# Kernel tuning notes

Hardware: AMD Instinct MI355X
Metric: run time of the kernel (lower is better)

## Reference

```python
import jax, jax.numpy as jnp
import numpy as np
import math

C = 256
GROUPS = 8
EPS = 1e-5

def setup_inputs() -> dict:
    key = jax.random.key(0)
    ks = jax.random.split(key, 10)
    b, c, h, w = 4, C, 64, 64
    x = jax.random.normal(ks[0], (b, c, h, w), dtype=jnp.float32)
    scale = 1.0 / math.sqrt(c)
    wq = jax.random.normal(ks[1], (c, c), dtype=jnp.float32) * scale
    wk = jax.random.normal(ks[2], (c, c), dtype=jnp.float32) * scale
    wv = jax.random.normal(ks[3], (c, c), dtype=jnp.float32) * scale
    wp = jax.random.normal(ks[4], (c, c), dtype=jnp.float32) * scale
    bq = jnp.zeros((c,), jnp.float32)
    bk = jnp.zeros((c,), jnp.float32)
    bv = jnp.zeros((c,), jnp.float32)
    bp = jnp.zeros((c,), jnp.float32)
    gamma = jnp.ones((c,), jnp.float32)
    beta = jnp.zeros((c,), jnp.float32)
    return {"x": x, "gamma": gamma, "beta": beta, "wq": wq, "bq": bq,
            "wk": wk, "bk": bk, "wv": wv, "bv": bv, "wp": wp, "bp": bp}

def _group_norm(x, gamma, beta):
    b, c, h, w = x.shape
    xr = x.reshape(b, GROUPS, c // GROUPS, h, w)
    mean = xr.mean(axis=(2, 3, 4), keepdims=True)
    var = xr.var(axis=(2, 3, 4), keepdims=True)
    xn = ((xr - mean) * jax.lax.rsqrt(var + EPS)).reshape(b, c, h, w)
    return xn * gamma[None, :, None, None] + beta[None, :, None, None]

def _conv1x1(x, w, bias):
    # 1x1 conv == channel matmul: [b,c,h,w] x [out,in] -> [b,out,h,w]
    return jnp.einsum('bchw,dc->bdhw', x, w) + bias[None, :, None, None]

def reference(x, gamma, beta, wq, bq, wk, bk, wv, bv, wp, bp):
    b, c, h, w = x.shape
    residual = x
    xn = _group_norm(x, gamma, beta)
    q = _conv1x1(xn, wq, bq).reshape(b, c, h * w).transpose(0, 2, 1)  # [b, hw, c]
    k = _conv1x1(xn, wk, bk).reshape(b, c, h * w)                    # [b, c, hw]
    v = _conv1x1(xn, wv, bv).reshape(b, c, h * w).transpose(0, 2, 1)  # [b, hw, c]
    attn = jnp.einsum('bqc,bck->bqk', q, k) / jnp.sqrt(jnp.float32(c))
    attn = jax.nn.softmax(attn, axis=-1)
    out = jnp.einsum('bqk,bkc->bqc', attn, v)                         # [b, hw, c]
    out = out.transpose(0, 2, 1).reshape(b, c, h, w)
    out = _conv1x1(out, wp, bp)
    return out + residual
```

## Files before the change

### kernel.cpp

```cpp
#include <hip/hip_runtime.h>

#define HW 4096
#define CD 256
#define KB 32
#define NKB 32
#define NSP 4
#define C1 0.09016844f

typedef __bf16 bf16x8v __attribute__((ext_vector_type(8)));
typedef float f32x4 __attribute__((ext_vector_type(4)));
typedef unsigned short u16;
typedef unsigned int u32;
typedef u16 u16x4 __attribute__((ext_vector_type(4)));
typedef u16 u16x8 __attribute__((ext_vector_type(8)));

static __device__ __forceinline__ u16 f2bf(float f){
  __bf16 h = (__bf16)f;
  return __builtin_bit_cast(u16, h);
}
static __device__ __forceinline__ float bf2f(u16 v){
  u32 u = ((u32)v) << 16;
  return __builtin_bit_cast(float, u);
}

static __device__ __forceinline__ f32x4 MFMA(u16x8 a, u16x8 b, f32x4 c){
  return __builtin_amdgcn_mfma_f32_16x16x32_bf16(
      __builtin_bit_cast(bf16x8v, a), __builtin_bit_cast(bf16x8v, b), c, 0, 0, 0);
}

#define GLL16(gsrc, ldst) __builtin_amdgcn_global_load_lds( \
    (const __attribute__((address_space(1))) void*)(gsrc),  \
    (__attribute__((address_space(3))) void*)(ldst), 16, 0, 0)

__global__ void k_prep(const float* __restrict__ wq, const float* __restrict__ wk,
                       const float* __restrict__ wv, const float* __restrict__ wp,
                       u16* __restrict__ Wbf){
  int z = blockIdx.y;
  const float* src = (z==0)?wq:(z==1)?wk:(z==2)?wv:wp;
  int i = (blockIdx.x*256 + threadIdx.x)*4;
  float4 v = *(const float4*)(src + i);
  u16x4 o = { f2bf(v.x), f2bf(v.y), f2bf(v.z), f2bf(v.w) };
  *(u16x4*)(Wbf + z*65536 + i) = o;
}

__global__ void k_gn1(const float* __restrict__ x, float* __restrict__ gpart){
  int g = blockIdx.x, b = blockIdx.y, ck = blockIdx.z;
  int tid = threadIdx.x;
  const float* xp = x + ((size_t)(b*CD) + g*32)*HW + ck*512;
  float s0 = 0.f, s1 = 0.f;
  #pragma unroll
  for (int j = 0; j < 16; ++j){
    int idx = j*1024 + tid*4;
    float4 v = *(const float4*)(xp + (size_t)(idx >> 9)*HW + (idx & 511));
    s0 += v.x + v.y + v.z + v.w;
    s1 += v.x*v.x + v.y*v.y + v.z*v.z + v.w*v.w;
  }
  #pragma unroll
  for (int m = 1; m < 64; m <<= 1){ s0 += __shfl_xor(s0, m); s1 += __shfl_xor(s1, m); }
  __shared__ float red[8];
  int lane = tid & 63, wave = tid >> 6;
  if (lane == 0){ red[wave] = s0; red[4+wave] = s1; }
  __syncthreads();
  if (tid == 0){
    float* dst = gpart + ((b*8 + g)*8 + ck)*2;
    dst[0] = red[0]+red[1]+red[2]+red[3];
    dst[1] = red[4]+red[5]+red[6]+red[7];
  }
}

__global__ void k_gn2(const float* __restrict__ x, const float* __restrict__ gamma,
                      const float* __restrict__ beta, const float* __restrict__ gpart,
                      u16* __restrict__ xnT){
  int g = blockIdx.x, b = blockIdx.y, ck = blockIdx.z;
  int tid = threadIdx.x;
  float s0 = 0.f, s1 = 0.f;
  #pragma unroll
  for (int s = 0; s < 8; ++s){
    const float* p = gpart + ((b*8 + g)*8 + s)*2;
    s0 += p[0]; s1 += p[1];
  }
  float inv_n = 1.0f/(32.0f*HW);
  float mean = s0*inv_n;
  float var = s1*inv_n - mean*mean;
  float rstd = rsqrtf(var + 1e-5f);
  int pl = tid >> 2, c8 = (tid & 3)*8;
  float av[8], bv_[8];
  #pragma unroll
  for (int e = 0; e < 8; ++e){
    int c = g*32 + c8 + e;
    float a = rstd * gamma[c];
    av[e] = a;
    bv_[e] = beta[c] - mean*a;
  }
  const float* xb = x + (size_t)(b*CD + g*32 + c8)*HW;
  #pragma unroll
  for (int it = 0; it < 8; ++it){
    int p = ck*512 + it*64 + pl;
    u16x8 o;
    #pragma unroll
    for (int e = 0; e < 8; ++e){
      float v = xb[(size_t)e*HW + p];
      o[e] = f2bf(v*av[e] + bv_[e]);
    }
    *(u16x8*)(xnT + ((size_t)(b*HW) + p)*CD + g*32 + c8) = o;
  }
}

__global__ __launch_bounds__(256,2) void k_qkv(const u16* __restrict__ xnT, const u16* __restrict__ Wbf,
    const float* __restrict__ bq, const float* __restrict__ bk, const float* __restrict__ bv,
    u16* __restrict__ Q, u16* __restrict__ K, u16* __restrict__ V){
  __shared__ u16 tile[4][4096];
  int z = blockIdx.z, b = blockIdx.y, pbase = blockIdx.x*64;
  int tid = threadIdx.x, lane = tid & 63, wave = tid >> 6;
  int lq = lane & 15, lg = lane >> 4;
  const u16* W = Wbf + z*65536;
  const float* bias = (z==0)?bq:(z==1)?bk:bv;
  int nbase = wave*64;
  f32x4 acc[4][4] = {};
  #pragma unroll
  for (int kk = 0; kk < 8; ++kk){
    u16x8 af[4], bf[4];
    #pragma unroll
    for (int m = 0; m < 4; ++m)
      af[m] = *(const u16x8*)(xnT + ((size_t)(b*HW + pbase + m*16 + lq))*CD + kk*32 + lg*8);
    #pragma unroll
    for (int n = 0; n < 4; ++n)
      bf[n] = *(const u16x8*)(W + (size_t)(nbase + n*16 + lq)*CD + kk*32 + lg*8);
    #pragma unroll
    for (int m = 0; m < 4; ++m)
      #pragma unroll
      for (int n = 0; n < 4; ++n)
        acc[m][n] = MFMA(af[m], bf[n], acc[m][n]);
  }
  #pragma unroll
  for (int n = 0; n < 4; ++n){
    float bb = bias[nbase + n*16 + lq];
    #pragma unroll
    for (int m = 0; m < 4; ++m){
      acc[m][n][0] += bb; acc[m][n][1] += bb; acc[m][n][2] += bb; acc[m][n][3] += bb;
    }
  }
  if (z == 2){
    #pragma unroll
    for (int m = 0; m < 4; ++m)
      #pragma unroll
      for (int n = 0; n < 4; ++n){
        int d = nbase + n*16 + lq;
        int p0 = pbase + m*16 + lg*4;
        u16x4 o = { f2bf(acc[m][n][0]), f2bf(acc[m][n][1]), f2bf(acc[m][n][2]), f2bf(acc[m][n][3]) };
        *(u16x4*)(V + (size_t)(b*CD + d)*HW + p0) = o;
      }
  } else {
    u16* dst = (z==0)?Q:K;
    u16* tl = tile[wave];
    #pragma unroll
    for (int m = 0; m < 4; ++m)
      #pragma unroll
      for (int n = 0; n < 4; ++n)
        #pragma unroll
        for (int r = 0; r < 4; ++r){
          int row = m*16 + lg*4 + r;
          int col = n*16 + lq;
          tl[row*64 + ((((col>>3) + row) & 7)<<3) + (col & 7)] = f2bf(acc[m][n][r]);
        }
    #pragma unroll
    for (int j = 0; j < 8; ++j){
      int idx = j*64 + lane;
      int row = idx >> 3, ch = idx & 7;
      u16x8 v = *(const u16x8*)(tl + row*64 + (((ch + row)&7)<<3));
      *(u16x8*)(dst + ((size_t)(b*HW + pbase + row))*CD + nbase + ch*8) = v;
    }
  }
}

__global__ __launch_bounds__(256,3) void k_attn(const u16* __restrict__ Q, const u16* __restrict__ K,
    const u16* __restrict__ V, u16* __restrict__ Opart, float2* __restrict__ ml){
  extern __shared__ char smem[];
  int tid = threadIdx.x, lane = tid & 63, wave = tid >> 6;
  int lq = lane & 15, lg = lane >> 4;
  int qt = blockIdx.x, sp = blockIdx.y, b = blockIdx.z;
  int qbase = qt*64 + wave*16;
  int key0 = sp*(NKB*KB);

  int ke[4], ve[4];
  #pragma unroll
  for (int i = 0; i < 4; ++i){
    int G = i*256 + tid;
    int kr = G >> 5;
    ke[i] = kr*CD + (((G & 31) ^ kr) & 31)*8;
    int vrow = G >> 3;
    int p = (G >> 2) & 1;
    int j = ((G & 3) - vrow) & 3;
    ve[i] = (vrow*2 + p)*HW + j*8;
  }
  int bvo = (lq>>1)*128 + (((lq&1)*4 + ((lg + (lq>>1)) & 3)))*16;

  u16x8 qa[8];
  #pragma unroll
  for (int cc = 0; cc < 8; ++cc)
    qa[cc] = *(const u16x8*)(Q + ((size_t)(b*HW + qbase + lq))*CD + cc*32 + lg*8);

  f32x4 o[16] = {};
  float m_ = -3.0e38f, l_ = 0.f;

  const u16* Kb = K + (size_t)(b*HW + key0)*CD;
  const u16* Vb = V + (size_t)(b*CD)*HW + key0;
  char* vd = smem + 32768;
  char* Pw = smem + 49152 + wave*1024;

  {
    char* kd = smem;
    #pragma unroll
    for (int i = 0; i < 4; ++i){
      GLL16(Kb + ke[i], kd + i*4096 + wave*1024);
      GLL16(Vb + ve[i], vd + i*4096 + wave*1024);
    }
  }
  __syncthreads();
  int cur = 0;
  for (int kb = 0; kb < NKB; ++kb){
    if (kb + 1 < NKB){
      char* kd = smem + (cur^1)*16384;
      const u16* kg = Kb + (size_t)(kb+1)*KB*CD;
      #pragma unroll
      for (int i = 0; i < 4; ++i)
        GLL16(kg + ke[i], kd + i*4096 + wave*1024);
    }
    const char* kt = smem + cur*16384;

    f32x4 sa[2];
    sa[0] = (f32x4){0.f,0.f,0.f,0.f};
    sa[1] = (f32x4){0.f,0.f,0.f,0.f};
    #pragma unroll
    for (int nt = 0; nt < 2; ++nt){
      int row = nt*16 + lq;
      #pragma unroll
      for (int cc = 0; cc < 8; ++cc){
        int ch = cc*4 + lg;
        u16x8 kf = *(const u16x8*)(kt + row*512 + (((ch ^ row) & 31) << 4));
        sa[nt] = MFMA(kf, qa[cc], sa[nt]);
      }
    }
    float v = fmaxf(fmaxf(fmaxf(sa[0][0], sa[0][1]), fmaxf(sa[0][2], sa[0][3])),
                    fmaxf(fmaxf(sa[1][0], sa[1][1]), fmaxf(sa[1][2], sa[1][3]))) * C1;
    v = fmaxf(v, __shfl_xor(v, 16));
    v = fmaxf(v, __shfl_xor(v, 32));
    if (!__all(v <= m_ + 8.0f)){
      float nm = fmaxf(m_, v);
      float corr = exp2f(m_ - nm);
      m_ = nm;
      l_ *= corr;
      float cr[4];
      #pragma unroll
      for (int r = 0; r < 4; ++r)
        cr[r] = __shfl(corr, lg*4 + r);
      #pragma unroll
      for (int nf = 0; nf < 16; ++nf)
        #pragma unroll
        for (int r = 0; r < 4; ++r)
          o[nf][r] *= cr[r];
    }
    float rs = 0.f;
    u32 pw[4];
    #pragma unroll
    for (int w = 0; w < 4; ++w){
      int nt = w >> 1, rr = w & 1;
      float p0 = exp2f(sa[nt][2*rr]  *C1 - m_);
      float p1 = exp2f(sa[nt][2*rr+1]*C1 - m_);
      rs += p0 + p1;
      pw[w] = (u32)f2bf(p0) | ((u32)f2bf(p1) << 16);
    }
    rs += __shfl_xor(rs, 16);
    rs += __shfl_xor(rs, 32);
    l_ += rs;
    #pragma unroll
    for (int w = 0; w < 4; ++w){
      int chunk = 2*(w>>1) + (lg>>1);
      int slot  = (chunk + (lq>>1)) & 3;
      int addr  = (lq>>1)*128 + ((lq&1)*4 + slot)*16 + ((2*lg + (w&1))&3)*4;
      *(u32*)(Pw + addr) = pw[w];
    }
    __syncthreads();
    u16x8 pa = *(const u16x8*)(Pw + bvo);
    #pragma unroll
    for (int nf = 0; nf < 16; ++nf){
      u16x8 vf = *(const u16x8*)(vd + nf*1024 + bvo);
      o[nf] = MFMA(pa, vf, o[nf]);
    }
    __syncthreads();
    if (kb + 1 < NKB){
      const u16* vg = Vb + (kb+1)*KB;
      #pragma unroll
      for (int i = 0; i < 4; ++i)
        GLL16(vg + ve[i], vd + i*4096 + wave*1024);
    }
    cur ^= 1;
  }
  size_t ob = ((size_t)((sp*4 + b)*HW + qbase))*CD;
  #pragma unroll
  for (int nf = 0; nf < 16; ++nf){
    int c = nf*16 + lq;
    #pragma unroll
    for (int r = 0; r < 4; ++r){
      int qq = lg*4 + r;
      Opart[ob + (size_t)qq*CD + c] = f2bf(o[nf][r]);
    }
  }
  if (lg == 0){
    ml[(size_t)(sp*4 + b)*HW + qbase + lq] = make_float2(m_, l_);
  }
}

__global__ void k_comb(const u16* __restrict__ Opart, const float2* __restrict__ ml,
                       u16* __restrict__ Opm){
  int b = blockIdx.y;
  int q = blockIdx.x*8 + (threadIdx.x >> 5);
  int c0 = (threadIdx.x & 31)*8;
  float2 e[NSP];
  float m = -3.0e38f;
  #pragma unroll
  for (int s = 0; s < NSP; ++s){
    e[s] = ml[(size_t)(s*4 + b)*HW + q];
    m = fmaxf(m, e[s].x);
  }
  float w[NSP], den = 0.f;
  #pragma unroll
  for (int s = 0; s < NSP; ++s){
    w[s] = exp2f(e[s].x - m);
    den += e[s].y * w[s];
  }
  float inv = 1.0f / den;
  float sum[8] = {};
  #pragma unroll
  for (int s = 0; s < NSP; ++s){
    u16x8 v = *(const u16x8*)(Opart + ((size_t)((s*4 + b)*HW) + q)*CD + c0);
    float ws = w[s];
    #pragma unroll
    for (int t = 0; t < 8; ++t)
      sum[t] += bf2f(v[t]) * ws;
  }
  u16x8 o;
  #pragma unroll
  for (int t = 0; t < 8; ++t)
    o[t] = f2bf(sum[t]*inv);
  *(u16x8*)(Opm + ((size_t)(b*HW) + q)*CD + c0) = o;
}

__global__ __launch_bounds__(256,2) void k_proj(const u16* __restrict__ Opm, const u16* __restrict__ Wp,
    const float* __restrict__ bp, const float* __restrict__ x, float* __restrict__ out){
  int b = blockIdx.y, pbase = blockIdx.x*64;
  int tid = threadIdx.x, lane = tid & 63, wave = tid >> 6;
  int lq = lane & 15, lg = lane >> 4;
  int nbase = wave*64;
  f32x4 acc[4][4] = {};
  #pragma unroll
  for (int kk = 0; kk < 8; ++kk){
    u16x8 af[4], bf[4];
    #pragma unroll
    for (int m = 0; m < 4; ++m)
      af[m] = *(const u16x8*)(Opm + ((size_t)(b*HW + pbase + m*16 + lq))*CD + kk*32 + lg*8);
    #pragma unroll
    for (int n = 0; n < 4; ++n)
      bf[n] = *(const u16x8*)(Wp + (size_t)(nbase + n*16 + lq)*CD + kk*32 + lg*8);
    #pragma unroll
    for (int m = 0; m < 4; ++m)
      #pragma unroll
      for (int n = 0; n < 4; ++n)
        acc[m][n] = MFMA(af[m], bf[n], acc[m][n]);
  }
  #pragma unroll
  for (int m = 0; m < 4; ++m)
    #pragma unroll
    for (int n = 0; n < 4; ++n){
      int d = nbase + n*16 + lq;
      int p0 = pbase + m*16 + lg*4;
      size_t base = (size_t)(b*CD + d)*HW + p0;
      float bb = bp[d];
      float4 res = *(const float4*)(x + base);
      float4 ov;
      ov.x = acc[m][n][0] + bb + res.x;
      ov.y = acc[m][n][1] + bb + res.y;
      ov.z = acc[m][n][2] + bb + res.z;
      ov.w = acc[m][n][3] + bb + res.w;
      *(float4*)(out + base) = ov;
    }
}

extern "C" void kernel_launch(void* const* d_in, const int* in_sizes, int n_in,
                              void* d_out, int out_size, void* d_ws, size_t ws_size,
                              hipStream_t stream){
  const float* x     = (const float*)d_in[0];
  const float* gamma = (const float*)d_in[1];
  const float* beta  = (const float*)d_in[2];
  const float* wq    = (const float*)d_in[3];
  const float* bq    = (const float*)d_in[4];
  const float* wk    = (const float*)d_in[5];
  const float* bk    = (const float*)d_in[6];
  const float* wv    = (const float*)d_in[7];
  const float* bv    = (const float*)d_in[8];
  const float* wp    = (const float*)d_in[9];
  const float* bp    = (const float*)d_in[10];
  float* out = (float*)d_out;

  char* ws = (char*)d_ws;
  u16*   xnT   = (u16*)(ws);
  u16*   Qb    = (u16*)(ws + (8ull<<20));
  u16*   Kb    = (u16*)(ws + (16ull<<20));
  u16*   Vb    = (u16*)(ws + (24ull<<20));
  u16*   Opm   = (u16*)(ws + (32ull<<20));
  u16*   Wbf   = (u16*)(ws + (40ull<<20));
  float2* mlb  = (float2*)(ws + (40ull<<20) + (512ull<<10));
  u16*   Opart = (u16*)(ws + (41ull<<20));
  float* gpart = (float*)Qb;

  hipFuncSetAttribute((const void*)k_attn, hipFuncAttributeMaxDynamicSharedMemorySize, 53248);

  k_prep<<<dim3(64,4), 256, 0, stream>>>(wq, wk, wv, wp, Wbf);
  k_gn1 <<<dim3(8,4,8), 256, 0, stream>>>(x, gpart);
  k_gn2 <<<dim3(8,4,8), 256, 0, stream>>>(x, gamma, beta, gpart, xnT);
  k_qkv <<<dim3(64,4,3), 256, 0, stream>>>(xnT, Wbf, bq, bk, bv, Qb, Kb, Vb);
  k_attn<<<dim3(64,NSP,4), 256, 53248, stream>>>(Qb, Kb, Vb, Opart, mlb);
  k_comb<<<dim3(512,4), 256, 0, stream>>>(Opart, mlb, Opm);
  k_proj<<<dim3(64,4), 256, 0, stream>>>(Opm, Wbf + 3*65536, bp, x, out);
}
```

Before: 187.9 us.

## Split attention work across wave pairs with double-buffered V and deferred rescale

The attention kernel moves from 256 to 512 threads. Each pair of waves shares 16 queries, with one wave handling half of every 32-key block for QK^T and half of the 256 output channels for PV. V is now double-buffered alongside K, so each iteration needs one barrier instead of two. The running-max rescale is deferred until after the PV MFMAs, using a row max shared through LDS and a lazy threshold starting from m=0. This halves per-wave accumulator registers and raises waves per CU, at the cost of more LDS per block, cross-wave max/sum exchange, and some overflow risk if early scores are far above zero.

```diff
diff --git a/kernel.cpp b/kernel.cpp
--- a/kernel.cpp
+++ b/kernel.cpp
@@ -173,19 +173,20 @@
   }
 }
 
-__global__ __launch_bounds__(256,3) void k_attn(const u16* __restrict__ Q, const u16* __restrict__ K,
+__global__ __launch_bounds__(512,4) void k_attn(const u16* __restrict__ Q, const u16* __restrict__ K,
     const u16* __restrict__ V, u16* __restrict__ Opart, float2* __restrict__ ml){
   extern __shared__ char smem[];
   int tid = threadIdx.x, lane = tid & 63, wave = tid >> 6;
   int lq = lane & 15, lg = lane >> 4;
+  int pair = wave >> 1, half = wave & 1;
   int qt = blockIdx.x, sp = blockIdx.y, b = blockIdx.z;
-  int qbase = qt*64 + wave*16;
+  int qbase = qt*64 + pair*16;
   int key0 = sp*(NKB*KB);
 
-  int ke[4], ve[4];
-  #pragma unroll
-  for (int i = 0; i < 4; ++i){
-    int G = i*256 + tid;
+  int ke[2], ve[2];
+  #pragma unroll
+  for (int i = 0; i < 2; ++i){
+    int G = i*512 + tid;
     int kr = G >> 5;
     ke[i] = kr*CD + (((G & 31) ^ kr) & 31)*8;
     int vrow = G >> 3;
@@ -200,20 +201,20 @@
   for (int cc = 0; cc < 8; ++cc)
     qa[cc] = *(const u16x8*)(Q + ((size_t)(b*HW + qbase + lq))*CD + cc*32 + lg*8);
 
-  f32x4 o[16] = {};
-  float m_ = -3.0e38f, l_ = 0.f;
+  f32x4 o[8] = {};
+  float m_ = 0.f, l_ = 0.f;
 
   const u16* Kb = K + (size_t)(b*HW + key0)*CD;
   const u16* Vb = V + (size_t)(b*CD)*HW + key0;
-  char* vd = smem + 32768;
-  char* Pw = smem + 49152 + wave*1024;
+  char* Pw = smem + 65536 + pair*1024;
+  float* mb = (float*)(smem + 69632);
 
   {
-    char* kd = smem;
-    #pragma unroll
-    for (int i = 0; i < 4; ++i){
-      GLL16(Kb + ke[i], kd + i*4096 + wave*1024);
-      GLL16(Vb + ve[i], vd + i*4096 + wave*1024);
+    char* kd = smem; char* vd = smem + 32768;
+    #pragma unroll
+    for (int i = 0; i < 2; ++i){
+      GLL16(Kb + ke[i], kd + i*8192 + wave*1024);
+      GLL16(Vb + ve[i], vd + i*8192 + wave*1024);
     }
   }
   __syncthreads();
@@ -223,30 +224,58 @@
       char* kd = smem + (cur^1)*16384;
       const u16* kg = Kb + (size_t)(kb+1)*KB*CD;
       #pragma unroll
-      for (int i = 0; i < 4; ++i)
-        GLL16(kg + ke[i], kd + i*4096 + wave*1024);
+      for (int i = 0; i < 2; ++i)
+        GLL16(kg + ke[i], kd + i*8192 + wave*1024);
     }
     const char* kt = smem + cur*16384;
 
-    f32x4 sa[2];
-    sa[0] = (f32x4){0.f,0.f,0.f,0.f};
-    sa[1] = (f32x4){0.f,0.f,0.f,0.f};
-    #pragma unroll
-    for (int nt = 0; nt < 2; ++nt){
-      int row = nt*16 + lq;
-      #pragma unroll
-      for (int cc = 0; cc < 8; ++cc){
-        int ch = cc*4 + lg;
-        u16x8 kf = *(const u16x8*)(kt + row*512 + (((ch ^ row) & 31) << 4));
-        sa[nt] = MFMA(kf, qa[cc], sa[nt]);
-      }
-    }
-    float v = fmaxf(fmaxf(fmaxf(sa[0][0], sa[0][1]), fmaxf(sa[0][2], sa[0][3])),
-                    fmaxf(fmaxf(sa[1][0], sa[1][1]), fmaxf(sa[1][2], sa[1][3]))) * C1;
+    f32x4 sa = (f32x4){0.f,0.f,0.f,0.f};
+    int row = half*16 + lq;
+    #pragma unroll
+    for (int cc = 0; cc < 8; ++cc){
+      int ch = cc*4 + lg;
+      u16x8 kf = *(const u16x8*)(kt + row*512 + (((ch ^ row) & 31) << 4));
+      sa = MFMA(kf, qa[cc], sa);
+    }
+    float t0 = sa[0]*C1, t1 = sa[1]*C1, t2 = sa[2]*C1, t3 = sa[3]*C1;
+    float v = fmaxf(fmaxf(t0, t1), fmaxf(t2, t3));
     v = fmaxf(v, __shfl_xor(v, 16));
     v = fmaxf(v, __shfl_xor(v, 32));
-    if (!__all(v <= m_ + 8.0f)){
-      float nm = fmaxf(m_, v);
+    if (lg == 0) mb[pair*32 + half*16 + lq] = v;
+    float rs;
+    {
+      float p0 = exp2f(t0 - m_), p1 = exp2f(t1 - m_);
+      float p2 = exp2f(t2 - m_), p3 = exp2f(t3 - m_);
+      rs = (p0 + p1) + (p2 + p3);
+      u32 w0 = (u32)f2bf(p0) | ((u32)f2bf(p1) << 16);
+      u32 w1 = (u32)f2bf(p2) | ((u32)f2bf(p3) << 16);
+      int chunk = 2*half + (lg>>1);
+      int slot  = (chunk + (lq>>1)) & 3;
+      int base  = (lq>>1)*128 + ((lq&1)*4 + slot)*16;
+      *(u32*)(Pw + base + ((2*lg + 0)&3)*4) = w0;
+      *(u32*)(Pw + base + ((2*lg + 1)&3)*4) = w1;
+    }
+    rs += __shfl_xor(rs, 16);
+    rs += __shfl_xor(rs, 32);
+    l_ += rs;
+    __syncthreads();
+    if (kb + 1 < NKB){
+      char* vd = smem + 32768 + (cur^1)*16384;
+      const u16* vg = Vb + (kb+1)*KB;
+      #pragma unroll
+      for (int i = 0; i < 2; ++i)
+        GLL16(vg + ve[i], vd + i*8192 + wave*1024);
+    }
+    float mx = fmaxf(mb[pair*32 + lq], mb[pair*32 + 16 + lq]);
+    u16x8 pa = *(const u16x8*)(Pw + bvo);
+    const char* vt = smem + 32768 + cur*16384;
+    #pragma unroll
+    for (int f = 0; f < 8; ++f){
+      u16x8 vf = *(const u16x8*)(vt + (half*8 + f)*1024 + bvo);
+      o[f] = MFMA(pa, vf, o[f]);
+    }
+    if (!__all(mx <= m_ + 8.0f)){
+      float nm = fmaxf(m_, mx);
       float corr = exp2f(m_ - nm);
       m_ = nm;
       l_ *= corr;
@@ -255,60 +284,27 @@
       for (int r = 0; r < 4; ++r)
         cr[r] = __shfl(corr, lg*4 + r);
       #pragma unroll
-      for (int nf = 0; nf < 16; ++nf)
+      for (int f = 0; f < 8; ++f)
         #pragma unroll
         for (int r = 0; r < 4; ++r)
-          o[nf][r] *= cr[r];
-    }
-    float rs = 0.f;
-    u32 pw[4];
-    #pragma unroll
-    for (int w = 0; w < 4; ++w){
-      int nt = w >> 1, rr = w & 1;
-      float p0 = exp2f(sa[nt][2*rr]  *C1 - m_);
-      float p1 = exp2f(sa[nt][2*rr+1]*C1 - m_);
-      rs += p0 + p1;
-      pw[w] = (u32)f2bf(p0) | ((u32)f2bf(p1) << 16);
-    }
-    rs += __shfl_xor(rs, 16);
-    rs += __shfl_xor(rs, 32);
-    l_ += rs;
-    #pragma unroll
-    for (int w = 0; w < 4; ++w){
-      int chunk = 2*(w>>1) + (lg>>1);
-      int slot  = (chunk + (lq>>1)) & 3;
-      int addr  = (lq>>1)*128 + ((lq&1)*4 + slot)*16 + ((2*lg + (w&1))&3)*4;
-      *(u32*)(Pw + addr) = pw[w];
-    }
-    __syncthreads();
-    u16x8 pa = *(const u16x8*)(Pw + bvo);
-    #pragma unroll
-    for (int nf = 0; nf < 16; ++nf){
-      u16x8 vf = *(const u16x8*)(vd + nf*1024 + bvo);
-      o[nf] = MFMA(pa, vf, o[nf]);
-    }
-    __syncthreads();
-    if (kb + 1 < NKB){
-      const u16* vg = Vb + (kb+1)*KB;
-      #pragma unroll
-      for (int i = 0; i < 4; ++i)
-        GLL16(vg + ve[i], vd + i*4096 + wave*1024);
+          o[f][r] *= cr[r];
     }
     cur ^= 1;
   }
+  __syncthreads();
+  if (lg == 0) mb[pair*32 + half*16 + lq] = l_;
+  __syncthreads();
+  float l_tot = mb[pair*32 + lq] + mb[pair*32 + 16 + lq];
   size_t ob = ((size_t)((sp*4 + b)*HW + qbase))*CD;
   #pragma unroll
-  for (int nf = 0; nf < 16; ++nf){
-    int c = nf*16 + lq;
-    #pragma unroll
-    for (int r = 0; r < 4; ++r){
-      int qq = lg*4 + r;
-      Opart[ob + (size_t)qq*CD + c] = f2bf(o[nf][r]);
-    }
-  }
-  if (lg == 0){
-    ml[(size_t)(sp*4 + b)*HW + qbase + lq] = make_float2(m_, l_);
-  }
+  for (int f = 0; f < 8; ++f){
+    int c = (half*8 + f)*16 + lq;
+    #pragma unroll
+    for (int r = 0; r < 4; ++r)
+      Opart[ob + (size_t)(lg*4 + r)*CD + c] = f2bf(o[f][r]);
+  }
+  if (half == 0 && lg == 0)
+    ml[(size_t)(sp*4 + b)*HW + qbase + lq] = make_float2(m_, l_tot);
 }
 
 __global__ void k_comb(const u16* __restrict__ Opart, const float2* __restrict__ ml,
@@ -413,13 +409,13 @@
   u16*   Opart = (u16*)(ws + (41ull<<20));
   float* gpart = (float*)Qb;
 
-  hipFuncSetAttribute((const void*)k_attn, hipFuncAttributeMaxDynamicSharedMemorySize, 53248);
+  hipFuncSetAttribute((const void*)k_attn, hipFuncAttributeMaxDynamicSharedMemorySize, 70144);
 
   k_prep<<<dim3(64,4), 256, 0, stream>>>(wq, wk, wv, wp, Wbf);
   k_gn1 <<<dim3(8,4,8), 256, 0, stream>>>(x, gpart);
   k_gn2 <<<dim3(8,4,8), 256, 0, stream>>>(x, gamma, beta, gpart, xnT);
   k_qkv <<<dim3(64,4,3), 256, 0, stream>>>(xnT, Wbf, bq, bk, bv, Qb, Kb, Vb);
-  k_attn<<<dim3(64,NSP,4), 256, 53248, stream>>>(Qb, Kb, Vb, Opart, mlb);
+  k_attn<<<dim3(64,NSP,4), 512, 70144, stream>>>(Qb, Kb, Vb, Opart, mlb);
   k_comb<<<dim3(512,4), 256, 0, stream>>>(Opart, mlb, Opm);
   k_proj<<<dim3(64,4), 256, 0, stream>>>(Opm, Wbf + 3*65536, bp, x, out);
 }
```

Measured after the change: 171.2 us. 1.1x faster.
